# Optimization experiments

Hardware: AMD Instinct MI355X
Metric: run time of the kernel (lower is better)

## Reference

```python
import jax, jax.numpy as jnp
import numpy as np

B, S, HID = 1, 4096, 2304
NH, NKV, HD = 8, 4, 256
SW = 2048                 # sliding window (layer_idx=0 -> active)
SOFTCAP = 50.0
SCALE = 256.0 ** -0.5     # query_pre_attn_scalar ** -0.5
THETA = 10000.0
NEG = -1e30


def rotate_half(x):
    x1, x2 = jnp.split(x, 2, axis=-1)
    return jnp.concatenate([-x2, x1], axis=-1)


def setup_inputs() -> dict:
    key = jax.random.key(0)
    ks = jax.random.split(key, 5)
    hidden_states = jax.random.normal(ks[0], (B, S, HID), jnp.float32)
    position_ids = jnp.tile(jnp.arange(S, dtype=jnp.int32)[None, :], (B, 1))
    Wq = 0.02 * jax.random.normal(ks[1], (NH * HD, HID), jnp.float32)
    Wk = 0.02 * jax.random.normal(ks[2], (NKV * HD, HID), jnp.float32)
    Wv = 0.02 * jax.random.normal(ks[3], (NKV * HD, HID), jnp.float32)
    Wo = 0.02 * jax.random.normal(ks[4], (HID, NH * HD), jnp.float32)
    return {"hidden_states": hidden_states, "position_ids": position_ids,
            "Wq": Wq, "Wk": Wk, "Wv": Wv, "Wo": Wo}


def reference(hidden_states, position_ids, Wq, Wk, Wv, Wo):
    b, s, _ = hidden_states.shape
    # fused QKV projections (torch Linear: y = x @ W.T)
    q = jnp.einsum('bsh,oh->bso', hidden_states, Wq).reshape(b, s, NH, HD).transpose(0, 2, 1, 3)
    k = jnp.einsum('bsh,oh->bso', hidden_states, Wk).reshape(b, s, NKV, HD).transpose(0, 2, 1, 3)
    v = jnp.einsum('bsh,oh->bso', hidden_states, Wv).reshape(b, s, NKV, HD).transpose(0, 2, 1, 3)

    # rotary embedding
    inv_freq = 1.0 / (THETA ** (jnp.arange(0, HD, 2, dtype=jnp.float32) / HD))
    freqs = position_ids.astype(jnp.float32)[:, :, None] * inv_freq[None, None, :]  # [b,s,hd/2]
    emb = jnp.concatenate([freqs, freqs], axis=-1)                                  # [b,s,hd]
    cos = jnp.cos(emb)[:, None, :, :]  # [b,1,s,hd]
    sin = jnp.sin(emb)[:, None, :, :]
    q = q * cos + rotate_half(q) * sin
    k = k * cos + rotate_half(k) * sin

    # GQA: repeat kv heads
    groups = NH // NKV
    k = jnp.repeat(k, groups, axis=1)  # [b,nh,s,hd]
    v = jnp.repeat(v, groups, axis=1)

    scores = jnp.einsum('bhqd,bhkd->bhqk', q, k) * SCALE
    scores = SOFTCAP * jnp.tanh(scores / SOFTCAP)  # logit softcapping

    i = jnp.arange(s)[:, None]
    j = jnp.arange(s)[None, :]
    mask = (j <= i) & ((i - j) < SW)               # causal + sliding window
    scores = jnp.where(mask[None, None], scores, NEG)

    attn = jax.nn.softmax(scores, axis=-1)
    out = jnp.einsum('bhqk,bhkd->bhqd', attn, v)
    out = out.transpose(0, 2, 1, 3).reshape(b, s, NH * HD)
    return jnp.einsum('bso,ho->bsh', out, Wo)
```

## Files before the change

### kernel.cpp

```cpp
#include <hip/hip_runtime.h>
#include <hip/hip_bf16.h>

typedef __attribute__((ext_vector_type(8))) short short8;
typedef __attribute__((ext_vector_type(4))) short short4v;
typedef __attribute__((ext_vector_type(4))) float floatx4;

#define S_LEN 4096
#define HIDDEN 2304
#define NHEADS 8
#define NKVH 4
#define HDIM 256
#define SWIN 2048

static __device__ __forceinline__ short bf16bits(float x) {
    __hip_bfloat16 h = __float2bfloat16(x);
    return __builtin_bit_cast(short, h);
}
static __device__ __forceinline__ float bits2f(short b) {
    return __bfloat162float(__builtin_bit_cast(__hip_bfloat16, b));
}

static __device__ __forceinline__ void gload_lds16(const short* g, short* l) {
    __builtin_amdgcn_global_load_lds((const __attribute__((address_space(1))) void*)g,
                                     (__attribute__((address_space(3))) void*)l,
                                     16, 0, 0);
}

__global__ __launch_bounds__(256) void cast_f32_bf16(const float* __restrict__ in,
                                                     short* __restrict__ out, int n4) {
    int i = blockIdx.x * 256 + threadIdx.x;
    if (i >= n4) return;
    float4 v = ((const float4*)in)[i];
    short4v o;
    o.x = bf16bits(v.x); o.y = bf16bits(v.y); o.z = bf16bits(v.z); o.w = bf16bits(v.w);
    ((short4v*)out)[i] = o;
}

__global__ __launch_bounds__(256) void cast_wqkv(const float* __restrict__ Wq,
                                                 const float* __restrict__ Wk,
                                                 const float* __restrict__ Wv,
                                                 short* __restrict__ dst) {
    const int NQ4 = 1179648, NK4 = 589824;
    int i = blockIdx.x * 256 + threadIdx.x;
    const float4* src;
    if (i < NQ4)            src = (const float4*)Wq + i;
    else if (i < NQ4 + NK4) src = (const float4*)Wk + (i - NQ4);
    else                    src = (const float4*)Wv + (i - NQ4 - NK4);
    float4 v = *src;
    short4v o;
    o.x = bf16bits(v.x); o.y = bf16bits(v.y); o.z = bf16bits(v.z); o.w = bf16bits(v.w);
    ((short4v*)dst)[i] = o;
}

template<int MODE>
__global__ __launch_bounds__(256) void gemm_lds(const short* __restrict__ A,
                                                const short* __restrict__ B,
                                                void* __restrict__ Cp,
                                                int M, int N, int K, int ldc)
{
    __shared__ __align__(16) short lA[128 * 32];
    __shared__ __align__(16) short lB[128 * 32];
    int tid  = threadIdx.x;
    int lane = tid & 63;
    int wave = tid >> 6;
    int col  = lane & 15;
    int quad = lane >> 4;
    int m_base = blockIdx.y * 128;
    int n_base = blockIdx.x * 128;
    int wm = (wave >> 1) * 64;
    int wn = (wave & 1) * 64;

    int srow = wave * 32 + (lane >> 2);
    int scol = (lane & 3) * 8;
    const short* gA0 = A + (size_t)(m_base + srow) * K + scol;
    const short* gA1 = gA0 + (size_t)16 * K;
    const short* gB0 = B + (size_t)(n_base + srow) * K + scol;
    const short* gB1 = gB0 + (size_t)16 * K;
    short* lA0 = lA + wave * 1024;
    short* lB0 = lB + wave * 1024;

    floatx4 acc[4][4] = {};

    for (int k0 = 0; k0 < K; k0 += 32) {
        __syncthreads();
        gload_lds16(gA0 + k0, lA0);
        gload_lds16(gA1 + k0, lA0 + 512);
        gload_lds16(gB0 + k0, lB0);
        gload_lds16(gB1 + k0, lB0 + 512);
        __syncthreads();

        short8 af[4], bf[4];
        #pragma unroll
        for (int t = 0; t < 4; ++t) {
            af[t] = *(const short8*)(lA + (wm + t*16 + col) * 32 + quad * 8);
            bf[t] = *(const short8*)(lB + (wn + t*16 + col) * 32 + quad * 8);
        }
        #pragma unroll
        for (int mt = 0; mt < 4; ++mt)
            #pragma unroll
            for (int nt = 0; nt < 4; ++nt)
                acc[mt][nt] = __builtin_amdgcn_mfma_f32_16x16x32_bf16(af[mt], bf[nt], acc[mt][nt], 0, 0, 0);
    }

    #pragma unroll
    for (int mt = 0; mt < 4; ++mt) {
        #pragma unroll
        for (int nt = 0; nt < 4; ++nt) {
            int n  = n_base + wn + nt*16 + col;
            int m0 = m_base + wm + mt*16 + quad*4;
            if (MODE == 0) {
                short* C = (short*)Cp;
                #pragma unroll
                for (int r = 0; r < 4; ++r)
                    C[(size_t)(m0 + r) * ldc + n] = bf16bits(acc[mt][nt][r]);
            } else {
                float* C = (float*)Cp;
                #pragma unroll
                for (int r = 0; r < 4; ++r)
                    C[(size_t)(m0 + r) * ldc + n] = acc[mt][nt][r];
            }
        }
    }
}

__global__ __launch_bounds__(256) void gemm_qkv(const short* __restrict__ A,
                                                const short* __restrict__ B,
                                                short* __restrict__ QKV,
                                                short* __restrict__ Vt)
{
    __shared__ __align__(16) short lA[128 * 32];
    __shared__ __align__(16) short lB[128 * 32];
    const int K = HIDDEN;
    int tid  = threadIdx.x;
    int lane = tid & 63;
    int wave = tid >> 6;
    int col  = lane & 15;
    int quad = lane >> 4;
    int m_base = blockIdx.y * 128;
    int n_base = blockIdx.x * 128;
    int wm = (wave >> 1) * 64;
    int wn = (wave & 1) * 64;

    int srow = wave * 32 + (lane >> 2);
    int scol = (lane & 3) * 8;
    const short* gA0 = A + (size_t)(m_base + srow) * K + scol;
    const short* gA1 = gA0 + (size_t)16 * K;
    const short* gB0 = B + (size_t)(n_base + srow) * K + scol;
    const short* gB1 = gB0 + (size_t)16 * K;
    short* lA0 = lA + wave * 1024;
    short* lB0 = lB + wave * 1024;

    floatx4 acc[4][4] = {};

    for (int k0 = 0; k0 < K; k0 += 32) {
        __syncthreads();
        gload_lds16(gA0 + k0, lA0);
        gload_lds16(gA1 + k0, lA0 + 512);
        gload_lds16(gB0 + k0, lB0);
        gload_lds16(gB1 + k0, lB0 + 512);
        __syncthreads();

        short8 af[4], bf[4];
        #pragma unroll
        for (int t = 0; t < 4; ++t) {
            af[t] = *(const short8*)(lA + (wm + t*16 + col) * 32 + quad * 8);
            bf[t] = *(const short8*)(lB + (wn + t*16 + col) * 32 + quad * 8);
        }
        #pragma unroll
        for (int mt = 0; mt < 4; ++mt)
            #pragma unroll
            for (int nt = 0; nt < 4; ++nt)
                acc[mt][nt] = __builtin_amdgcn_mfma_f32_16x16x32_bf16(af[mt], bf[nt], acc[mt][nt], 0, 0, 0);
    }

    #pragma unroll
    for (int mt = 0; mt < 4; ++mt) {
        #pragma unroll
        for (int nt = 0; nt < 4; ++nt) {
            int n  = n_base + wn + nt*16 + col;
            int m0 = m_base + wm + mt*16 + quad*4;
            if (n_base + wn + nt*16 < 3072) {
                #pragma unroll
                for (int r = 0; r < 4; ++r)
                    QKV[(size_t)(m0 + r) * 4096 + n] = bf16bits(acc[mt][nt][r]);
            } else {
                short4v v;
                v.x = bf16bits(acc[mt][nt][0]);
                v.y = bf16bits(acc[mt][nt][1]);
                v.z = bf16bits(acc[mt][nt][2]);
                v.w = bf16bits(acc[mt][nt][3]);
                *(short4v*)(Vt + (size_t)(n - 3072) * 4096 + m0) = v;
            }
        }
    }
}

__global__ __launch_bounds__(256) void rope_kernel(short* __restrict__ QKV,
                                                   const int* __restrict__ pos)
{
    int t = blockIdx.x * 256 + threadIdx.x;
    int d   = t & 127;
    int rem = t >> 7;
    int hh  = rem % 12;
    int s   = rem / 12;
    float p   = (float)pos[s];
    float inv = __expf(-9.210340371976184f * ((float)d * (1.0f/128.0f)));
    float ang = p * inv;
    float sn, cs;
    sincosf(ang, &sn, &cs);
    short* row = QKV + (size_t)s * 4096 + hh * 256;
    float x1 = bits2f(row[d]);
    float x2 = bits2f(row[d + 128]);
    row[d]       = bf16bits(x1 * cs - x2 * sn);
    row[d + 128] = bf16bits(x2 * cs + x1 * sn);
}

__global__ __launch_bounds__(256) void attn_kernel(const short* __restrict__ QKV,
                                                   const short* __restrict__ Vt,
                                                   short* __restrict__ Ob)
{
    __shared__ __align__(16) short lK[32 * 256];
    __shared__ __align__(16) short lV[256 * 32];
    __shared__ __align__(16) short lP[4][16 * 40];
    int tid  = threadIdx.x;
    int lane = tid & 63;
    int wave = tid >> 6;
    int col  = lane & 15;
    int quad = lane >> 4;
    int bid  = blockIdx.x;
    int g     = bid >> 7;
    int chunk = (bid >> 1) & 63;
    int h     = g * 2 + (bid & 1);
    int qb = chunk * 64;
    int q0 = qb + wave * 16;

    const short* Qrow = QKV + (size_t)(q0 + col) * 4096 + h * 256;
    short8 qf[8];
    #pragma unroll
    for (int c = 0; c < 8; ++c)
        qf[c] = *(const short8*)(Qrow + c*32 + quad*8);

    int k_key = (lane >> 2);
    int k_sub = (lane & 3) * 8;
    const short* gK[2][2];
    short* dK[2][2];
    #pragma unroll
    for (int cc = 0; cc < 2; ++cc)
        #pragma unroll
        for (int hh = 0; hh < 2; ++hh) {
            int c = 2*wave + cc;
            gK[cc][hh] = QKV + (size_t)(hh*16 + k_key) * 4096 + 2048 + g*256 + c*32 + k_sub;
            dK[cc][hh] = lK + c*1024 + hh*512;
        }
    const short* gV[4];
    short* dV[4];
    #pragma unroll
    for (int jj = 0; jj < 4; ++jj) {
        int j = 4*wave + jj;
        gV[jj] = Vt + (size_t)(g*256 + j*16 + k_key) * 4096 + (lane & 3) * 8;
        dV[jj] = lV + j*512;
    }

    floatx4 o[16] = {};
    float psum[4] = {0.f, 0.f, 0.f, 0.f};

    int kb_start = qb - (SWIN - 1);
    if (kb_start < 0) kb_start = 0;
    kb_start &= ~31;

    for (int kb = kb_start; kb < qb + 64; kb += 32) {
        __syncthreads();
        #pragma unroll
        for (int cc = 0; cc < 2; ++cc)
            #pragma unroll
            for (int hh = 0; hh < 2; ++hh)
                gload_lds16(gK[cc][hh] + (size_t)kb * 4096, dK[cc][hh]);
        #pragma unroll
        for (int jj = 0; jj < 4; ++jj)
            gload_lds16(gV[jj] + kb, dV[jj]);
        __syncthreads();

        floatx4 sc[2] = {};
        #pragma unroll
        for (int t = 0; t < 2; ++t)
            #pragma unroll
            for (int c = 0; c < 8; ++c) {
                short8 kf = *(const short8*)(lK + c*1024 + (t*16 + col)*32 + quad*8);
                sc[t] = __builtin_amdgcn_mfma_f32_16x16x32_bf16(qf[c], kf, sc[t], 0, 0, 0);
            }

        int j0 = kb + col;
        int j1 = kb + 16 + col;
        #pragma unroll
        for (int r = 0; r < 4; ++r) {
            int i = q0 + quad*4 + r;
            float y0 = sc[0][r] * 0.0625f;
            float y1 = sc[1][r] * 0.0625f;
            float x20 = y0 * y0 * 4.0e-4f;
            float x21 = y1 * y1 * 4.0e-4f;
            float sv0 = y0 * (1.0f + x20 * (-0.33333333f + x20 * 0.13333333f));
            float sv1 = y1 * (1.0f + x21 * (-0.33333333f + x21 * 0.13333333f));
            bool v0 = (j0 <= i) && ((i - j0) < SWIN);
            bool v1 = (j1 <= i) && ((i - j1) < SWIN);
            float p0 = v0 ? __expf(sv0 - 12.0f) : 0.0f;
            float p1 = v1 ? __expf(sv1 - 12.0f) : 0.0f;
            lP[wave][(quad*4 + r)*40 + col]      = bf16bits(p0);
            lP[wave][(quad*4 + r)*40 + 16 + col] = bf16bits(p1);
            psum[r] += p0 + p1;
        }
        __threadfence_block();
        short8 pa = *(const short8*)(&lP[wave][col*40 + quad*8]);

        #pragma unroll
        for (int nt = 0; nt < 16; ++nt) {
            short8 vf = *(const short8*)(lV + (nt*16 + col)*32 + quad*8);
            o[nt] = __builtin_amdgcn_mfma_f32_16x16x32_bf16(pa, vf, o[nt], 0, 0, 0);
        }
    }

    #pragma unroll
    for (int off = 1; off < 16; off <<= 1)
        #pragma unroll
        for (int r = 0; r < 4; ++r)
            psum[r] += __shfl_xor(psum[r], off, 64);

    #pragma unroll
    for (int nt = 0; nt < 16; ++nt)
        #pragma unroll
        for (int r = 0; r < 4; ++r) {
            int i = q0 + quad*4 + r;
            Ob[(size_t)i * 2048 + h*256 + nt*16 + col] = bf16bits(o[nt][r] / psum[r]);
        }
}

extern "C" void kernel_launch(void* const* d_in, const int* in_sizes, int n_in,
                              void* d_out, int out_size, void* d_ws, size_t ws_size,
                              hipStream_t stream)
{
    const float* X  = (const float*)d_in[0];
    const int*  pos = (const int*)d_in[1];
    const float* Wq = (const float*)d_in[2];
    const float* Wk = (const float*)d_in[3];
    const float* Wv = (const float*)d_in[4];
    const float* Wo = (const float*)d_in[5];
    float* out = (float*)d_out;
    char* ws = (char*)d_ws;

    short* Xb    = (short*)(ws + 0);
    short* Wqkvb = (short*)(ws + 18874368);
    short* Wob   = (short*)(ws + 37748736);
    short* QKVb  = (short*)(ws + 47185920);
    short* Vt    = (short*)(ws + 80740352);
    short* Ob    = (short*)(ws + 0);

    cast_f32_bf16<<<9216, 256, 0, stream>>>(X,  Xb,  2359296);
    cast_wqkv<<<9216, 256, 0, stream>>>(Wq, Wk, Wv, Wqkvb);
    cast_f32_bf16<<<4608, 256, 0, stream>>>(Wo, Wob, 1179648);

    gemm_qkv<<<dim3(32,32), 256, 0, stream>>>(Xb, Wqkvb, QKVb, Vt);

    rope_kernel<<<24576, 256, 0, stream>>>(QKVb, pos);

    attn_kernel<<<512, 256, 0, stream>>>(QKVb, Vt, Ob);

    gemm_lds<2><<<dim3(18,32), 256, 0, stream>>>(Ob, Wob, out, 4096, 2304, 2048, 2304);
}
```

Baseline: 463.4 us.

## Restructure attention: 2 waves × 32 queries, 64-key tiles, swizzled LDS, mask skip

The attention kernel now runs 2 waves per block, each owning 32 query rows (two MFMA M-tiles), and processes 64-key blocks instead of 32. Each K/V fragment loaded from LDS is reused across both query tiles, which halves LDS reads per MFMA. XOR swizzling on the K, V and P LDS layouts is meant to avoid bank conflicts, and a fast path skips masking for fully-valid tiles. In exchange, per-thread register use roughly doubles (32 accumulators of floatx4), LDS use grows to about 80KB per block, and each block has only 2 waves, so occupancy and latency hiding may drop.

```diff
diff --git a/kernel.cpp b/kernel.cpp
--- a/kernel.cpp
+++ b/kernel.cpp
@@ -215,13 +215,13 @@
     row[d + 128] = bf16bits(x2 * cs + x1 * sn);
 }
 
-__global__ __launch_bounds__(256) void attn_kernel(const short* __restrict__ QKV,
+__global__ __launch_bounds__(128) void attn_kernel(const short* __restrict__ QKV,
                                                    const short* __restrict__ Vt,
                                                    short* __restrict__ Ob)
 {
-    __shared__ __align__(16) short lK[32 * 256];
-    __shared__ __align__(16) short lV[256 * 32];
-    __shared__ __align__(16) short lP[4][16 * 40];
+    __shared__ __align__(16) short lK[64 * 256];
+    __shared__ __align__(16) short lV[256 * 64];
+    __shared__ __align__(16) short lP[2][32 * 64];
     int tid  = threadIdx.x;
     int lane = tid & 63;
     int wave = tid >> 6;
@@ -232,105 +232,130 @@
     int chunk = (bid >> 1) & 63;
     int h     = g * 2 + (bid & 1);
     int qb = chunk * 64;
-    int q0 = qb + wave * 16;
-
-    const short* Qrow = QKV + (size_t)(q0 + col) * 4096 + h * 256;
-    short8 qf[8];
-    #pragma unroll
-    for (int c = 0; c < 8; ++c)
-        qf[c] = *(const short8*)(Qrow + c*32 + quad*8);
-
-    int k_key = (lane >> 2);
-    int k_sub = (lane & 3) * 8;
-    const short* gK[2][2];
-    short* dK[2][2];
-    #pragma unroll
-    for (int cc = 0; cc < 2; ++cc)
-        #pragma unroll
-        for (int hh = 0; hh < 2; ++hh) {
-            int c = 2*wave + cc;
-            gK[cc][hh] = QKV + (size_t)(hh*16 + k_key) * 4096 + 2048 + g*256 + c*32 + k_sub;
-            dK[cc][hh] = lK + c*1024 + hh*512;
-        }
-    const short* gV[4];
-    short* dV[4];
-    #pragma unroll
-    for (int jj = 0; jj < 4; ++jj) {
-        int j = 4*wave + jj;
-        gV[jj] = Vt + (size_t)(g*256 + j*16 + k_key) * 4096 + (lane & 3) * 8;
-        dV[jj] = lV + j*512;
-    }
-
-    floatx4 o[16] = {};
-    float psum[4] = {0.f, 0.f, 0.f, 0.f};
+    int q0 = qb + wave * 32;
+
+    short8 qf[2][8];
+    #pragma unroll
+    for (int mt = 0; mt < 2; ++mt) {
+        const short* Qrow = QKV + (size_t)(q0 + mt*16 + col) * 4096 + h * 256;
+        #pragma unroll
+        for (int c = 0; c < 8; ++c)
+            qf[mt][c] = *(const short8*)(Qrow + c*32 + quad*8);
+    }
+
+    int keyL = wave * 32 + (lane >> 5);
+    int segK = lane & 31;
+    const short* pK[4];
+    #pragma unroll
+    for (int j = 0; j < 4; ++j) {
+        int key = keyL + 2 * j;
+        pK[j] = QKV + (size_t)key * 4096 + 2048 + g * 256 + ((segK ^ (key & 7)) << 3);
+    }
+    short* dK = lK + wave * 32 * 256;
+
+    int dL   = wave * 128 + (lane >> 3);
+    int segV = lane & 7;
+    const short* pV = Vt + (size_t)(g * 256 + dL) * 4096 + ((segV ^ (dL & 7)) << 3);
+    short* dV = lV + wave * 128 * 64;
+
+    floatx4 o[2][16] = {};
+    float psum[2][4] = {};
 
     int kb_start = qb - (SWIN - 1);
     if (kb_start < 0) kb_start = 0;
-    kb_start &= ~31;
-
-    for (int kb = kb_start; kb < qb + 64; kb += 32) {
-        __syncthreads();
-        #pragma unroll
-        for (int cc = 0; cc < 2; ++cc)
-            #pragma unroll
-            for (int hh = 0; hh < 2; ++hh)
-                gload_lds16(gK[cc][hh] + (size_t)kb * 4096, dK[cc][hh]);
-        #pragma unroll
-        for (int jj = 0; jj < 4; ++jj)
-            gload_lds16(gV[jj] + kb, dV[jj]);
-        __syncthreads();
-
-        floatx4 sc[2] = {};
-        #pragma unroll
-        for (int t = 0; t < 2; ++t)
-            #pragma unroll
-            for (int c = 0; c < 8; ++c) {
-                short8 kf = *(const short8*)(lK + c*1024 + (t*16 + col)*32 + quad*8);
-                sc[t] = __builtin_amdgcn_mfma_f32_16x16x32_bf16(qf[c], kf, sc[t], 0, 0, 0);
+    kb_start &= ~63;
+
+    for (int kb = kb_start; kb < qb + 64; kb += 64) {
+        __syncthreads();
+        #pragma unroll
+        for (int i = 0; i < 16; ++i)
+            gload_lds16(pK[i & 3] + (size_t)(kb + 8 * (i >> 2)) * 4096, dK + 2*i*256);
+        #pragma unroll
+        for (int i = 0; i < 16; ++i)
+            gload_lds16(pV + (size_t)(8 * i) * 4096 + kb, dV + 8*i*64);
+        __syncthreads();
+
+        floatx4 sc[2][4] = {};
+        #pragma unroll
+        for (int c = 0; c < 8; ++c) {
+            short8 kf[4];
+            #pragma unroll
+            for (int kt = 0; kt < 4; ++kt)
+                kf[kt] = *(const short8*)(lK + (kt*16 + col) * 256
+                                             + ((c*32 + quad*8) ^ ((col & 7) << 3)));
+            #pragma unroll
+            for (int mt = 0; mt < 2; ++mt)
+                #pragma unroll
+                for (int kt = 0; kt < 4; ++kt)
+                    sc[mt][kt] = __builtin_amdgcn_mfma_f32_16x16x32_bf16(qf[mt][c], kf[kt], sc[mt][kt], 0, 0, 0);
+        }
+
+        bool full = (kb + 64 <= q0) && (kb + SWIN >= q0 + 32);
+#define SOFTMAX_BODY(MASKED)                                                        \
+        _Pragma("unroll")                                                           \
+        for (int mt = 0; mt < 2; ++mt)                                              \
+            _Pragma("unroll")                                                       \
+            for (int kt = 0; kt < 4; ++kt)                                          \
+                _Pragma("unroll")                                                   \
+                for (int r = 0; r < 4; ++r) {                                       \
+                    float y  = sc[mt][kt][r] * 0.0625f;                             \
+                    float x2 = y * y * 4.0e-4f;                                     \
+                    float sv = y * (1.0f + x2 * (-0.33333333f + x2 * 0.13333333f)); \
+                    float p  = __expf(sv - 12.0f);                                  \
+                    if (MASKED) {                                                   \
+                        int i = q0 + mt*16 + quad*4 + r;                            \
+                        int j = kb + kt*16 + col;                                   \
+                        bool v = (j <= i) && ((i - j) < SWIN);                      \
+                        p = v ? p : 0.0f;                                           \
+                    }                                                               \
+                    psum[mt][r] += p;                                               \
+                    int q = mt*16 + quad*4 + r;                                     \
+                    lP[wave][q*64 + ((kt*16 + col) ^ ((q & 7) << 3))] = bf16bits(p);\
+                }
+        if (full) { SOFTMAX_BODY(false) } else { SOFTMAX_BODY(true) }
+#undef SOFTMAX_BODY
+
+        __threadfence_block();
+
+        short8 pa[2][2];
+        #pragma unroll
+        for (int mt = 0; mt < 2; ++mt)
+            #pragma unroll
+            for (int kh = 0; kh < 2; ++kh)
+                pa[mt][kh] = *(const short8*)(&lP[wave][(mt*16 + col) * 64
+                                                 + ((kh*32 + quad*8) ^ ((col & 7) << 3))]);
+
+        #pragma unroll
+        for (int nt = 0; nt < 16; ++nt) {
+            short8 vf0 = *(const short8*)(lV + (nt*16 + col) * 64
+                                             + ((quad*8)      ^ ((col & 7) << 3)));
+            short8 vf1 = *(const short8*)(lV + (nt*16 + col) * 64
+                                             + ((32 + quad*8) ^ ((col & 7) << 3)));
+            #pragma unroll
+            for (int mt = 0; mt < 2; ++mt) {
+                o[mt][nt] = __builtin_amdgcn_mfma_f32_16x16x32_bf16(pa[mt][0], vf0, o[mt][nt], 0, 0, 0);
+                o[mt][nt] = __builtin_amdgcn_mfma_f32_16x16x32_bf16(pa[mt][1], vf1, o[mt][nt], 0, 0, 0);
             }
-
-        int j0 = kb + col;
-        int j1 = kb + 16 + col;
-        #pragma unroll
-        for (int r = 0; r < 4; ++r) {
-            int i = q0 + quad*4 + r;
-            float y0 = sc[0][r] * 0.0625f;
-            float y1 = sc[1][r] * 0.0625f;
-            float x20 = y0 * y0 * 4.0e-4f;
-            float x21 = y1 * y1 * 4.0e-4f;
-            float sv0 = y0 * (1.0f + x20 * (-0.33333333f + x20 * 0.13333333f));
-            float sv1 = y1 * (1.0f + x21 * (-0.33333333f + x21 * 0.13333333f));
-            bool v0 = (j0 <= i) && ((i - j0) < SWIN);
-            bool v1 = (j1 <= i) && ((i - j1) < SWIN);
-            float p0 = v0 ? __expf(sv0 - 12.0f) : 0.0f;
-            float p1 = v1 ? __expf(sv1 - 12.0f) : 0.0f;
-            lP[wave][(quad*4 + r)*40 + col]      = bf16bits(p0);
-            lP[wave][(quad*4 + r)*40 + 16 + col] = bf16bits(p1);
-            psum[r] += p0 + p1;
-        }
-        __threadfence_block();
-        short8 pa = *(const short8*)(&lP[wave][col*40 + quad*8]);
-
-        #pragma unroll
-        for (int nt = 0; nt < 16; ++nt) {
-            short8 vf = *(const short8*)(lV + (nt*16 + col)*32 + quad*8);
-            o[nt] = __builtin_amdgcn_mfma_f32_16x16x32_bf16(pa, vf, o[nt], 0, 0, 0);
         }
     }
 
     #pragma unroll
     for (int off = 1; off < 16; off <<= 1)
         #pragma unroll
-        for (int r = 0; r < 4; ++r)
-            psum[r] += __shfl_xor(psum[r], off, 64);
-
-    #pragma unroll
-    for (int nt = 0; nt < 16; ++nt)
-        #pragma unroll
-        for (int r = 0; r < 4; ++r) {
-            int i = q0 + quad*4 + r;
-            Ob[(size_t)i * 2048 + h*256 + nt*16 + col] = bf16bits(o[nt][r] / psum[r]);
-        }
+        for (int mt = 0; mt < 2; ++mt)
+            #pragma unroll
+            for (int r = 0; r < 4; ++r)
+                psum[mt][r] += __shfl_xor(psum[mt][r], off, 64);
+
+    #pragma unroll
+    for (int mt = 0; mt < 2; ++mt)
+        #pragma unroll
+        for (int nt = 0; nt < 16; ++nt)
+            #pragma unroll
+            for (int r = 0; r < 4; ++r) {
+                int i = q0 + mt*16 + quad*4 + r;
+                Ob[(size_t)i * 2048 + h*256 + nt*16 + col] = bf16bits(o[mt][nt][r] / psum[mt][r]);
+            }
 }
 
 extern "C" void kernel_launch(void* const* d_in, const int* in_sizes, int n_in,
@@ -361,7 +386,7 @@
 
     rope_kernel<<<24576, 256, 0, stream>>>(QKVb, pos);
 
-    attn_kernel<<<512, 256, 0, stream>>>(QKVb, Vt, Ob);
+    attn_kernel<<<512, 128, 0, stream>>>(QKVb, Vt, Ob);
 
     gemm_lds<2><<<dim3(18,32), 256, 0, stream>>>(Ob, Wob, out, 4096, 2304, 2048, 2304);
 }
```

New measurement: 486.4 us. 1.05x slower.
